# Kernel optimization log

Measured on AMD Instinct MI355X. Metric: run time of the kernel, lower is better.

## Reference

```python
import jax, jax.numpy as jnp
import numpy as np
import math
from jax import lax

CANVAS = 300.0
NUM_CLASSES = 80
SCORE_THR = 0.01
K_CAND = 400   # candidates kept per image before NMS (cfg cltop=400)
K_OUT = 200    # final detections per image
IOU_THR = 0.45
CLIP = math.log(1000.0 / 16.0)  # exp clamp in decode_boxes
_FSIZES = [38, 19, 10, 5, 3, 1]
_STRIDES = [8, 16, 32, 64, 100, 300]
_SCALES = [0.07, 0.15, 0.33, 0.51, 0.69, 0.87, 1.05]
_AR3 = [1, 2, 3]
_ANUMS = [4, 6, 6, 6, 4, 4]


def _make_priors():
    # SSD300 priors (tv config: no rounding, clamp to canvas), cxcywh, [8732,4]
    out = []
    for i, (st, fs) in enumerate(zip(_STRIDES, _FSIZES)):
        s = _SCALES[i] * 300.0
        e = math.sqrt(_SCALES[i] * _SCALES[i + 1]) * 300.0
        ratios = [2.0, 0.5] + ([3.0, 1.0 / 3.0] if i in _AR3 else [])
        wh = [(s, s), (e, e)] + [(s * math.sqrt(r), s / math.sqrt(r)) for r in ratios]
        wh = np.array([(min(w, 300.0), min(h, 300.0)) for w, h in wh], np.float32)
        cy, cx = np.meshgrid(np.arange(fs), np.arange(fs), indexing='ij')
        ctr = np.stack([(cx + 0.5) * st, (cy + 0.5) * st], -1).reshape(-1, 2).astype(np.float32)
        A = wh.shape[0]
        out.append(np.concatenate([np.repeat(ctr, A, 0), np.tile(wh, (fs * fs, 1))], 1))
    return np.concatenate(out, 0)


def _head(x, w, b, tl):
    # Conv2d(c, an*tl, 3, 1, 1) -> permute(0,2,3,1) -> reshape(B, -1, tl)
    y = lax.conv_general_dilated(x, w, (1, 1), [(1, 1), (1, 1)],
                                 dimension_numbers=('NCHW', 'OIHW', 'NCHW'))
    y = y + b[None, :, None, None]
    n = y.shape[0]
    return jnp.transpose(y, (0, 2, 3, 1)).reshape(n, -1, tl)


def _decode(deltas, pri):
    cx = pri[:, 0] + deltas[:, 0] * 0.1 * pri[:, 2]
    cy = pri[:, 1] + deltas[:, 1] * 0.1 * pri[:, 3]
    w = pri[:, 2] * jnp.exp(jnp.minimum(deltas[:, 2] * 0.2, CLIP))
    h = pri[:, 3] * jnp.exp(jnp.minimum(deltas[:, 3] * 0.2, CLIP))
    b = jnp.stack([cx - 0.5 * w, cy - 0.5 * h, cx + 0.5 * w, cy + 0.5 * h], -1)
    return jnp.clip(b, 0.0, CANVAS)  # clamp_to_canvas


def _pairwise_iou(b):
    area = (b[:, 2] - b[:, 0]) * (b[:, 3] - b[:, 1])
    lt = jnp.maximum(b[:, None, :2], b[None, :, :2])
    rb = jnp.minimum(b[:, None, 2:], b[None, :, 2:])
    wh = jnp.clip(rb - lt, 0.0)
    inter = wh[..., 0] * wh[..., 1]
    return inter / (area[:, None] + area[None, :] - inter + 1e-9)


def _post_one(scr, reg, priors):
    # scr [A, C] (background already dropped), reg [A, 4]
    C = scr.shape[1]
    flat = jnp.where(scr > SCORE_THR, scr, 0.0).reshape(-1)
    s, idx = lax.top_k(flat, K_CAND)          # sorted desc -> greedy NMS order
    cls = idx % C + 1                          # bckg_class_first=False -> +1
    anc = idx // C
    boxes = _decode(reg[anc], priors[anc])
    valid = (s > 0.0) & (boxes[:, 2] > boxes[:, 0]) & (boxes[:, 3] > boxes[:, 1])
    s = jnp.where(valid, s, 0.0)
    # class-aware NMS via per-class coordinate offset (batched_nms trick)
    off = cls.astype(boxes.dtype)[:, None] * (CANVAS + 1.0)
    iou = _pairwise_iou(boxes + off)
    def body(i, keep):
        sup = (iou[i] > IOU_THR) & (jnp.arange(K_CAND) > i) & keep[i]
        return keep & (~sup)
    keep = lax.fori_loop(0, K_CAND, body, valid)
    fs, fi = lax.top_k(jnp.where(keep, s, 0.0), K_OUT)
    return boxes[fi], fs, jnp.where(fs > 0.0, cls[fi], 0).astype(jnp.int32)


def setup_inputs() -> dict:
    key = jax.random.key(0)
    shapes = [(16, 512, 38, 38), (16, 1024, 19, 19), (16, 512, 10, 10),
              (16, 256, 5, 5), (16, 256, 3, 3), (16, 256, 1, 1)]
    d = {}
    k = key
    for i, (shp, an) in enumerate(zip(shapes, _ANUMS)):
        c = shp[1]
        k, k1, k2, k3 = jax.random.split(k, 4)
        d['feat%d' % i] = jax.random.normal(k1, shp, jnp.float32)
        d['cls_w%d' % i] = jax.random.normal(k2, (an * (NUM_CLASSES + 1), c, 3, 3), jnp.float32) * 0.03
        d['cls_b%d' % i] = jnp.zeros((an * (NUM_CLASSES + 1),), jnp.float32)
        d['reg_w%d' % i] = jax.random.normal(k3, (an * 4, c, 3, 3), jnp.float32) * 0.03
        d['reg_b%d' % i] = jnp.zeros((an * 4,), jnp.float32)
    d['priors'] = jnp.asarray(_make_priors())
    return d


def reference(feat0, feat1, feat2, feat3, feat4, feat5,
              cls_w0, cls_b0, cls_w1, cls_b1, cls_w2, cls_b2,
              cls_w3, cls_b3, cls_w4, cls_b4, cls_w5, cls_b5,
              reg_w0, reg_b0, reg_w1, reg_b1, reg_w2, reg_b2,
              reg_w3, reg_b3, reg_w4, reg_b4, reg_w5, reg_b5,
              priors):
    feats = [feat0, feat1, feat2, feat3, feat4, feat5]
    cws = [cls_w0, cls_w1, cls_w2, cls_w3, cls_w4, cls_w5]
    cbs = [cls_b0, cls_b1, cls_b2, cls_b3, cls_b4, cls_b5]
    rws = [reg_w0, reg_w1, reg_w2, reg_w3, reg_w4, reg_w5]
    rbs = [reg_b0, reg_b1, reg_b2, reg_b3, reg_b4, reg_b5]
    cls = jnp.concatenate([_head(f, w, b, NUM_CLASSES + 1) for f, w, b in zip(feats, cws, cbs)], 1)
    reg = jnp.concatenate([_head(f, w, b, 4) for f, w, b in zip(feats, rws, rbs)], 1)
    scr = jax.nn.softmax(cls, axis=-1)[:, :, 1:]  # drop background (class 0)
    boxes, scores, classes = jax.vmap(_post_one, in_axes=(0, 0, None))(scr, reg, priors)
    return boxes, scores, classes
```

## Files before the change

kernel.cpp:

```cpp
#include <hip/hip_runtime.h>
#include <math.h>
#include <stdint.h>

#define NIMG 16
#define A_TOTAL 8732
#define NCLS 80
#define TL_CLS 81
#define CANVASF 300.0f
#define SCORE_THR 0.01f
#define IOU_THRF 0.45f
#define KCAND 400
#define KOUT 200
#define CAND_CAP 4096
#define NBIN 65536

typedef double d4 __attribute__((ext_vector_type(4)));

__device__ __forceinline__ float clampf(float v, float lo, float hi) {
    return fminf(fmaxf(v, lo), hi);
}

struct ConvJobs {
    const float* feat[6];
    const float* wgtT[6];
    const float* biasC[6];
    const float* biasR[6];
    float* outc;
    float* outr;
    int Cin[6], lgC[6], Hd[6], Mtot[6], Mcls[6], Mp[6], an[6], off[6], cn[6];
    int mW[6], jobTiles[6];
    int cum[8][7];
    int cs[8][6];
};

struct TransJobs {
    const float* srcC[6];
    const float* srcR[6];
    float* dst[6];
    int Cin[6], K[6], Mcls[6], Mtot[6], Mp[6], mT[6], start[6];
    int total;
};

__global__ __launch_bounds__(256) void transpose_wgt(TransJobs tj)
{
    __shared__ float lds[32][33];
    int bid = (int)blockIdx.x;
    int L = 0;
    while (L + 1 < 6 && bid >= tj.start[L + 1]) L++;
    int rel = bid - tj.start[L];
    int mTi = rel % tj.mT[L];
    int kTi = rel / tj.mT[L];
    int m0 = mTi * 32, k0 = kTi * 32;
    const int K = tj.K[L];
    const int tid = threadIdx.x;

    {
        int ml = tid >> 3;
        int kq = (tid & 7) << 2;
        int m = m0 + ml;
        float4 v = make_float4(0.f, 0.f, 0.f, 0.f);
        if (m < tj.Mcls[L])
            v = *(const float4*)(tj.srcC[L] + (size_t)m * K + k0 + kq);
        else if (m < tj.Mtot[L])
            v = *(const float4*)(tj.srcR[L] + (size_t)(m - tj.Mcls[L]) * K + k0 + kq);
        lds[kq + 0][ml] = v.x;
        lds[kq + 1][ml] = v.y;
        lds[kq + 2][ml] = v.z;
        lds[kq + 3][ml] = v.w;
    }
    __syncthreads();
    {
        int kk = tid >> 3;
        int mq = (tid & 7) << 2;
        int k = k0 + kk;
        int ci = k / 9;
        int r = k - ci * 9;
        int kp = r * tj.Cin[L] + ci;
        float4 w;
        w.x = lds[kk][mq + 0];
        w.y = lds[kk][mq + 1];
        w.z = lds[kk][mq + 2];
        w.w = lds[kk][mq + 3];
        *(float4*)(tj.dst[L] + (size_t)kp * tj.Mp[L] + m0 + mq) = w;
    }
}

template<int CN>
__device__ __forceinline__ void conv_wave(
    const float* __restrict__ feat, const float* __restrict__ wgtT,
    const float* __restrict__ biasC, const float* __restrict__ biasR,
    float* __restrict__ outc, float* __restrict__ outr,
    int Cin, int lgC, int Hd, int Mtot, int Mcls, int Mp, int an, int lvl_off,
    int n0, int m0)
{
    const int K = Cin * 9;
    const int HW = Hd * Hd;
    const int N = NIMG * HW;
    const int CHW = Cin * HW;
    const int lane = threadIdx.x & 63;
    const int lm = lane & 15;
    const int lk = lane >> 4;

    int rowIdx[4], colIdx[4];
    {
        d4 z = (d4){0.0, 0.0, 0.0, 0.0};
        d4 pr = __builtin_amdgcn_mfma_f64_16x16x4f64((double)lm, 1.0, z, 0, 0, 0);
        d4 pc = __builtin_amdgcn_mfma_f64_16x16x4f64(1.0, (double)lm, z, 0, 0, 0);
#pragma unroll
        for (int i = 0; i < 4; i++) {
            rowIdx[i] = (int)(pr[i] * 0.25 + 0.5);
            colIdx[i] = (int)(pc[i] * 0.25 + 0.5);
        }
    }

    const int gPerR = Cin >> 2;
    const int KBg = K >> 2;

    int voffA = lk * Mp + m0 + lm;
    int voffB[CN];
    float maskc[CN];
    float bufA[2][2], bufB[2][CN], bufM[2][CN];

    d4 acc[2][CN];
#pragma unroll
    for (int a = 0; a < 2; a++)
#pragma unroll
        for (int c = 0; c < CN; c++) acc[a][c] = (d4){0.0, 0.0, 0.0, 0.0};

    auto newR = [&](int r) {
        int ky = (r * 171) >> 9;
        int kx = r - 3 * ky;
#pragma unroll
        for (int c = 0; c < CN; c++) {
            int ng = n0 + lm + 16 * c;
            bool nv = ng < N;
            int bimg = 0, p = 0;
            if (nv) { bimg = ng / HW; p = ng - bimg * HW; }
            int y0 = p / Hd;
            int x0 = p - y0 * Hd;
            int yy = y0 + ky - 1;
            int xx = x0 + kx - 1;
            bool v = nv && (yy >= 0) && (yy < Hd) && (xx >= 0) && (xx < Hd);
            maskc[c] = v ? 1.0f : 0.0f;
            voffB[c] = bimg * CHW + lk * HW + (v ? (yy * Hd + xx) : 0);
        }
    };

    auto loadG = [&](int g, int slot) {
        if ((g & (gPerR - 1)) == 0) newR(g >> (lgC - 2));
#pragma unroll
        for (int c = 0; c < CN; c++) {
            bufB[slot][c] = feat[voffB[c]];
            bufM[slot][c] = maskc[c];
            voffB[c] += 4 * HW;
        }
        bufA[slot][0] = wgtT[voffA];
        bufA[slot][1] = wgtT[voffA + 16];
        voffA += 4 * Mp;
    };

    loadG(0, 0);
    loadG(1, 1);
    for (int g = 0; g < KBg; g += 2) {
        {
            double a0 = (double)bufA[0][0];
            double a1 = (double)bufA[0][1];
            double bb[CN];
#pragma unroll
            for (int c = 0; c < CN; c++) bb[c] = (double)(bufB[0][c] * bufM[0][c]);
            if (g + 2 < KBg) loadG(g + 2, 0);
#pragma unroll
            for (int c = 0; c < CN; c++) {
                acc[0][c] = __builtin_amdgcn_mfma_f64_16x16x4f64(a0, bb[c], acc[0][c], 0, 0, 0);
                acc[1][c] = __builtin_amdgcn_mfma_f64_16x16x4f64(a1, bb[c], acc[1][c], 0, 0, 0);
            }
        }
        {
            double a0 = (double)bufA[1][0];
            double a1 = (double)bufA[1][1];
            double bb[CN];
#pragma unroll
            for (int c = 0; c < CN; c++) bb[c] = (double)(bufB[1][c] * bufM[1][c]);
            if (g + 3 < KBg) loadG(g + 3, 1);
#pragma unroll
            for (int c = 0; c < CN; c++) {
                acc[0][c] = __builtin_amdgcn_mfma_f64_16x16x4f64(a0, bb[c], acc[0][c], 0, 0, 0);
                acc[1][c] = __builtin_amdgcn_mfma_f64_16x16x4f64(a1, bb[c], acc[1][c], 0, 0, 0);
            }
        }
    }

#pragma unroll
    for (int mi2 = 0; mi2 < 2; mi2++)
#pragma unroll
    for (int c = 0; c < CN; c++)
#pragma unroll
    for (int i = 0; i < 4; i++) {
        int mg = m0 + mi2 * 16 + rowIdx[i];
        int ng2 = n0 + c * 16 + colIdx[i];
        if (mg >= Mtot || ng2 >= N) continue;
        int b = ng2 / HW;
        int p = ng2 - b * HW;
        double val = acc[mi2][c][i];
        if (mg < Mcls) {
            int aidx = mg / TL_CLS;
            int t = mg - aidx * TL_CLS;
            int row = lvl_off + p * an + aidx;
            outc[((size_t)b * A_TOTAL + row) * TL_CLS + t] = (float)(val + (double)biasC[mg]);
        } else {
            int rm = mg - Mcls;
            int aidx = rm >> 2;
            int t = rm & 3;
            int row = lvl_off + p * an + aidx;
            outr[((size_t)b * A_TOTAL + row) * 4 + t] = (float)(val + (double)biasR[rm]);
        }
    }
}

__global__ __launch_bounds__(256, 4) void fused_conv(ConvJobs J)
{
    int bid = (int)blockIdx.x;
    int x = bid & 7;
    int r = bid >> 3;
    if (r >= J.cum[x][6]) return;
    int j = 0;
    while (j + 1 < 6 && r >= J.cum[x][j + 1]) j++;
    int blkInJob = J.cs[x][j] + (r - J.cum[x][j]);

    int wave = threadIdx.x >> 6;
    int tile = blkInJob * 4 + wave;
    if (tile >= J.jobTiles[j]) return;
    int mt = tile % J.mW[j];
    int nt = tile / J.mW[j];

    if (J.cn[j] == 2)
        conv_wave<2>(J.feat[j], J.wgtT[j], J.biasC[j], J.biasR[j], J.outc, J.outr,
                     J.Cin[j], J.lgC[j], J.Hd[j], J.Mtot[j], J.Mcls[j], J.Mp[j],
                     J.an[j], J.off[j], nt * 32, mt * 32);
    else
        conv_wave<4>(J.feat[j], J.wgtT[j], J.biasC[j], J.biasR[j], J.outc, J.outr,
                     J.Cin[j], J.lgC[j], J.Hd[j], J.Mtot[j], J.Mcls[j], J.Mp[j],
                     J.an[j], J.off[j], nt * 64, mt * 32);
}

__global__ __launch_bounds__(256) void softmax_kernel(
    const float* __restrict__ cls, float* __restrict__ scr, int nrows)
{
    __shared__ float buf[64 * 81];
    __shared__ float inv[64];
    const int row0 = blockIdx.x * 64;
    const int tid = threadIdx.x;

    for (int i = tid; i < 64 * 81; i += 256) {
        int r = row0 + i / 81;
        buf[i] = (r < nrows) ? cls[(size_t)row0 * 81 + i] : 0.0f;
    }
    __syncthreads();
    if (tid < 64) {
        float m = -1e30f;
        for (int c = 0; c < 81; c++) m = fmaxf(m, buf[tid * 81 + c]);
        double md = (double)m;
        double ssum = 0.0;
        for (int c = 0; c < 81; c++) {
            double e = exp((double)buf[tid * 81 + c] - md);
            buf[tid * 81 + c] = (float)e;
            ssum += e;
        }
        inv[tid] = (float)(1.0 / ssum);
    }
    __syncthreads();
    for (int i = tid; i < 64 * 80; i += 256) {
        int r = i / 80;
        int c = i - r * 80;
        int gr = row0 + r;
        if (gr < nrows) scr[(size_t)gr * 80 + c] = buf[r * 81 + c + 1] * inv[r];
    }
}

__global__ void zero_kernel(unsigned int* __restrict__ p, int n)
{
    int i = blockIdx.x * blockDim.x + threadIdx.x;
    if (i < n) p[i] = 0u;
}

__global__ void hist_kernel(const float* __restrict__ scr, unsigned int* __restrict__ hist)
{
    const int per_img = A_TOTAL * NCLS;
    const size_t total = (size_t)NIMG * per_img;
    for (size_t i = (size_t)blockIdx.x * blockDim.x + threadIdx.x; i < total;
         i += (size_t)gridDim.x * blockDim.x) {
        float v = scr[i];
        if (v > SCORE_THR) {
            int img = (int)(i / per_img);
            unsigned int u = __float_as_uint(v);
            atomicAdd(&hist[img * NBIN + (u >> 16)], 1u);
        }
    }
}

__global__ __launch_bounds__(1024) void select_kernel(
    const unsigned int* __restrict__ hist, unsigned int* __restrict__ sel)
{
    __shared__ unsigned int vals[1024];
    __shared__ unsigned int red[1024];
    __shared__ int s_total, s_b0, s_done;
    const int img = blockIdx.x;
    const int tid = threadIdx.x;
    if (tid == 0) { s_total = 0; s_b0 = 0; s_done = 0; }
    __syncthreads();
    for (int c = 63; c >= 0; c--) {
        unsigned int h = hist[img * NBIN + c * 1024 + tid];
        vals[tid] = h;
        red[tid] = h;
        __syncthreads();
        for (int s = 512; s > 0; s >>= 1) {
            if (tid < s) red[tid] += red[tid + s];
            __syncthreads();
        }
        if (tid == 0 && !s_done) {
            if (s_total + (int)red[0] >= KCAND) {
                int cum = s_total;
                for (int tt = 1023; tt >= 0; tt--) {
                    cum += (int)vals[tt];
                    if (cum >= KCAND) { s_b0 = c * 1024 + tt; s_done = 1; break; }
                }
            } else {
                s_total += (int)red[0];
            }
        }
        __syncthreads();
        if (s_done) break;
    }
    if (tid == 0) sel[img] = (unsigned int)s_b0;
}

__global__ void gather_kernel(const float* __restrict__ scr,
                              const unsigned int* __restrict__ sel,
                              unsigned int* __restrict__ candcnt,
                              uint2* __restrict__ cand)
{
    const int per_img = A_TOTAL * NCLS;
    const size_t total = (size_t)NIMG * per_img;
    for (size_t i = (size_t)blockIdx.x * blockDim.x + threadIdx.x; i < total;
         i += (size_t)gridDim.x * blockDim.x) {
        float v = scr[i];
        if (v > SCORE_THR) {
            int img = (int)(i / per_img);
            unsigned int u = __float_as_uint(v);
            if ((u >> 16) >= sel[img]) {
                unsigned int pos = atomicAdd(&candcnt[img], 1u);
                if (pos < CAND_CAP) {
                    unsigned int ridx = (unsigned int)(i - (size_t)img * per_img);
                    cand[(size_t)img * CAND_CAP + pos] = make_uint2(u, ridx);
                }
            }
        }
    }
}

__global__ __launch_bounds__(1024) void nms_kernel(
    const uint2* __restrict__ cand, const unsigned int* __restrict__ candcnt,
    const float* __restrict__ reg_all, const float* __restrict__ priors,
    float* __restrict__ out)
{
    __shared__ unsigned long long key[CAND_CAP];
    __shared__ float s_sc[KCAND];
    __shared__ float s_bx[KCAND][4];
    __shared__ float s_ob[KCAND][4];
    __shared__ float s_ar[KCAND];
    __shared__ float s_cl[KCAND];
    __shared__ int s_keep[KCAND];
    __shared__ int s_fi[KOUT];

    const int img = blockIdx.x;
    const int tid = threadIdx.x;
    unsigned int craw = candcnt[img];
    const int cnt = (craw > CAND_CAP) ? CAND_CAP : (int)craw;

    for (int i = tid; i < CAND_CAP; i += 1024) {
        unsigned long long kv = 0ull;
        if (i < cnt) {
            uint2 e = cand[(size_t)img * CAND_CAP + i];
            kv = ((unsigned long long)e.x << 32) | (unsigned int)(~e.y);
        }
        key[i] = kv;
    }
    __syncthreads();

    for (int ksz = 2; ksz <= CAND_CAP; ksz <<= 1) {
        for (int jj = ksz >> 1; jj > 0; jj >>= 1) {
            for (int i = tid; i < CAND_CAP; i += 1024) {
                int p = i ^ jj;
                if (p > i) {
                    bool desc = ((i & ksz) == 0);
                    unsigned long long a = key[i];
                    unsigned long long b = key[p];
                    bool sw = desc ? (a < b) : (a > b);
                    if (sw) { key[i] = b; key[p] = a; }
                }
            }
            __syncthreads();
        }
    }

    const float CLIPF = 4.135166556742356f;
    if (tid < KCAND) {
        const int j = tid;
        float s = 0.0f;
        unsigned int idx = 0u;
        if (j < cnt) {
            unsigned long long kv = key[j];
            unsigned int bits = (unsigned int)(kv >> 32);
            idx = ~((unsigned int)kv);
            s = __uint_as_float(bits);
        }
        int anc = (int)(idx / NCLS);
        int cl = (int)(idx - (unsigned int)anc * NCLS) + 1;
        const float* d = reg_all + ((size_t)img * A_TOTAL + anc) * 4;
        const float* pr = priors + (size_t)anc * 4;
        float d0 = d[0], d1 = d[1], d2 = d[2], d3 = d[3];
        float p0 = pr[0], p1 = pr[1], p2 = pr[2], p3 = pr[3];
        float cx = p0 + d0 * 0.1f * p2;
        float cy = p1 + d1 * 0.1f * p3;
        float t2 = fminf(d2 * 0.2f, CLIPF);
        float t3 = fminf(d3 * 0.2f, CLIPF);
        float bw = p2 * (float)exp((double)t2);
        float bh = p3 * (float)exp((double)t3);
        float x1 = clampf(cx - 0.5f * bw, 0.0f, CANVASF);
        float y1 = clampf(cy - 0.5f * bh, 0.0f, CANVASF);
        float x2 = clampf(cx + 0.5f * bw, 0.0f, CANVASF);
        float y2 = clampf(cy + 0.5f * bh, 0.0f, CANVASF);
        bool valid = (s > 0.0f) && (x2 > x1) && (y2 > y1);
        s = valid ? s : 0.0f;
        float off = (float)cl * (CANVASF + 1.0f);
        float ox1 = x1 + off, oy1 = y1 + off, ox2 = x2 + off, oy2 = y2 + off;
        s_sc[j] = s;
        s_cl[j] = (float)cl;
        s_keep[j] = valid ? 1 : 0;
        s_bx[j][0] = x1; s_bx[j][1] = y1; s_bx[j][2] = x2; s_bx[j][3] = y2;
        s_ob[j][0] = ox1; s_ob[j][1] = oy1; s_ob[j][2] = ox2; s_ob[j][3] = oy2;
        s_ar[j] = (ox2 - ox1) * (oy2 - oy1);
    }
    __syncthreads();

    for (int i = 0; i < KCAND; i++) {
        int ki = s_keep[i];
        if (ki && tid < KCAND && tid > i) {
            float lx = fmaxf(s_ob[i][0], s_ob[tid][0]);
            float ly = fmaxf(s_ob[i][1], s_ob[tid][1]);
            float rx = fminf(s_ob[i][2], s_ob[tid][2]);
            float ry = fminf(s_ob[i][3], s_ob[tid][3]);
            float iw = fmaxf(rx - lx, 0.0f);
            float ih = fmaxf(ry - ly, 0.0f);
            float inter = iw * ih;
            float iou = inter / (s_ar[i] + s_ar[tid] - inter + 1e-9f);
            if (iou > IOU_THRF) s_keep[tid] = 0;
        }
        __syncthreads();
    }

    if (tid == 0) {
        int pos = 0;
        for (int j = 0; j < KCAND && pos < KOUT; j++)
            if (s_keep[j]) s_fi[pos++] = j;
        for (int j = 0; j < KCAND && pos < KOUT; j++)
            if (!s_keep[j]) s_fi[pos++] = j;
    }
    __syncthreads();

    if (tid < KOUT) {
        int j = s_fi[tid];
        float fs = s_keep[j] ? s_sc[j] : 0.0f;
        size_t o = (size_t)img * KOUT + tid;
        out[o * 4 + 0] = s_bx[j][0];
        out[o * 4 + 1] = s_bx[j][1];
        out[o * 4 + 2] = s_bx[j][2];
        out[o * 4 + 3] = s_bx[j][3];
        out[(size_t)NIMG * KOUT * 4 + o] = fs;
        out[(size_t)NIMG * KOUT * 5 + o] = (fs > 0.0f) ? s_cl[j] : 0.0f;
    }
}

extern "C" void kernel_launch(void* const* d_in, const int* in_sizes, int n_in,
                              void* d_out, int out_size, void* d_ws, size_t ws_size,
                              hipStream_t stream)
{
    static const int Cin_[6] = {512, 1024, 512, 256, 256, 256};
    static const int lgC_[6] = {9, 10, 9, 8, 8, 8};
    static const int HW_[6]  = {38, 19, 10, 5, 3, 1};
    static const int an_[6]  = {4, 6, 6, 6, 4, 4};
    static const int off_[6] = {0, 5776, 7942, 8542, 8692, 8728};
    static const int Mp_[6]  = {352, 512, 512, 512, 352, 352};
    static const size_t wOffF_[6] = {0, 1622016, 6340608, 8699904, 0, 9879552};

    char* ws = (char*)d_ws;
    const size_t OFF_CLS  = 0;
    const size_t OFF_SCR  = 45266688;
    const size_t OFF_REG  = 89974528;
    const size_t OFF_HIST = 92209920;
    const size_t OFF_CCNT = 96404224;
    const size_t OFF_SEL  = 96404288;
    const size_t OFF_CAND = 96404352;

    float* cls_all = (float*)(ws + OFF_CLS);
    float* scr     = (float*)(ws + OFF_SCR);
    float* reg_all = (float*)(ws + OFF_REG);
    unsigned int* hist    = (unsigned int*)(ws + OFF_HIST);
    unsigned int* candcnt = (unsigned int*)(ws + OFF_CCNT);
    unsigned int* sel     = (unsigned int*)(ws + OFF_SEL);
    uint2* cand           = (uint2*)(ws + OFF_CAND);

    float* wT = scr;
    float* hT = (float*)hist;

    {
        TransJobs tj;
        int ts = 0;
        for (int L = 0; L < 6; L++) {
            tj.srcC[L] = (const float*)d_in[L * 5 + 1];
            tj.srcR[L] = (const float*)d_in[L * 5 + 3];
            tj.dst[L] = (L == 4) ? hT : (wT + wOffF_[L]);
            tj.Cin[L] = Cin_[L];
            tj.K[L] = Cin_[L] * 9;
            tj.Mcls[L] = an_[L] * TL_CLS;
            tj.Mtot[L] = an_[L] * 85;
            tj.Mp[L] = Mp_[L];
            tj.mT[L] = Mp_[L] / 32;
            tj.start[L] = ts;
            ts += (Mp_[L] / 32) * (Cin_[L] * 9 / 32);
        }
        tj.total = ts;
        transpose_wgt<<<ts, 256, 0, stream>>>(tj);
    }

    ConvJobs jobs;
    static const int ord_lvl[6] = {1, 0, 2, 3, 4, 5};
    int Bj[6];
    for (int q = 0; q < 6; q++) {
        int L = ord_lvl[q];
        int an = an_[L];
        jobs.feat[q]  = (const float*)d_in[L * 5 + 0];
        jobs.wgtT[q]  = (L == 4) ? hT : (wT + wOffF_[L]);
        jobs.biasC[q] = (const float*)d_in[L * 5 + 2];
        jobs.biasR[q] = (const float*)d_in[L * 5 + 4];
        jobs.Cin[q]   = Cin_[L];
        jobs.lgC[q]   = lgC_[L];
        jobs.Hd[q]    = HW_[L];
        jobs.Mcls[q]  = an * TL_CLS;
        jobs.Mtot[q]  = an * 85;
        jobs.Mp[q]    = Mp_[L];
        jobs.an[q]    = an;
        jobs.off[q]   = off_[L];
        jobs.cn[q]    = (L == 1) ? 2 : 4;
        int N = NIMG * HW_[L] * HW_[L];
        int nstep = 16 * jobs.cn[q];
        int nT = (N + nstep - 1) / nstep;
        int mW = (jobs.Mtot[q] + 31) / 32;
        jobs.mW[q] = mW;
        jobs.jobTiles[q] = nT * mW;
        Bj[q] = (nT * mW + 3) / 4;
    }
    int maxT = 0;
    for (int x = 0; x < 8; x++) {
        int acc = 0;
        for (int q = 0; q < 6; q++) {
            int s = (int)(((long long)x * Bj[q]) / 8);
            int e = (int)(((long long)(x + 1) * Bj[q]) / 8);
            jobs.cs[x][q] = s;
            jobs.cum[x][q] = acc;
            acc += e - s;
        }
        jobs.cum[x][6] = acc;
        if (acc > maxT) maxT = acc;
    }
    jobs.outc = cls_all;
    jobs.outr = reg_all;

    fused_conv<<<8 * maxT, 256, 0, stream>>>(jobs);

    {
        int nz = NIMG * NBIN + 16 + 16;
        zero_kernel<<<(nz + 255) / 256, 256, 0, stream>>>(hist, nz);
    }

    softmax_kernel<<<(NIMG * A_TOTAL + 63) / 64, 256, 0, stream>>>(cls_all, scr, NIMG * A_TOTAL);
    hist_kernel<<<2048, 256, 0, stream>>>(scr, hist);
    select_kernel<<<NIMG, 1024, 0, stream>>>(hist, sel);
    gather_kernel<<<2048, 256, 0, stream>>>(scr, sel, candcnt, cand);
    nms_kernel<<<NIMG, 1024, 0, stream>>>(cand, candcnt, reg_all,
                                          (const float*)d_in[30], (float*)d_out);
}
```

Baseline: 3.769 ms.

## Reorder conv weight K layout, fuse histogram into softmax, parallelize select scan

```diff
diff --git a/kernel.cpp b/kernel.cpp
--- a/kernel.cpp
+++ b/kernel.cpp
@@ -27,7 +27,7 @@
     const float* biasR[6];
     float* outc;
     float* outr;
-    int Cin[6], lgC[6], Hd[6], Mtot[6], Mcls[6], Mp[6], an[6], off[6], cn[6];
+    int Cin[6], Hd[6], Mtot[6], Mcls[6], Mp[6], an[6], off[6], cn[6];
     int mW[6], jobTiles[6];
     int cum[8][7];
     int cs[8][6];
@@ -75,7 +75,7 @@
         int k = k0 + kk;
         int ci = k / 9;
         int r = k - ci * 9;
-        int kp = r * tj.Cin[L] + ci;
+        int kp = (ci >> 2) * 36 + r * 4 + (ci & 3);
         float4 w;
         w.x = lds[kk][mq + 0];
         w.y = lds[kk][mq + 1];
@@ -90,10 +90,9 @@
     const float* __restrict__ feat, const float* __restrict__ wgtT,
     const float* __restrict__ biasC, const float* __restrict__ biasR,
     float* __restrict__ outc, float* __restrict__ outr,
-    int Cin, int lgC, int Hd, int Mtot, int Mcls, int Mp, int an, int lvl_off,
+    int Cin, int Hd, int Mtot, int Mcls, int Mp, int an, int lvl_off,
     int n0, int m0)
 {
-    const int K = Cin * 9;
     const int HW = Hd * Hd;
     const int N = NIMG * HW;
     const int CHW = Cin * HW;
@@ -113,82 +112,90 @@
         }
     }
 
-    const int gPerR = Cin >> 2;
-    const int KBg = K >> 2;
+    int voffB[CN];
+    int bits[CN];
+#pragma unroll
+    for (int c = 0; c < CN; c++) {
+        int ng = n0 + lm + 16 * c;
+        bool nv = ng < N;
+        int bimg = 0, p = 0;
+        if (nv) { bimg = ng / HW; p = ng - bimg * HW; }
+        int y0 = p / Hd;
+        int x0 = p - y0 * Hd;
+        voffB[c] = nv ? (bimg * CHW + lk * HW + y0 * Hd + x0) : 0;
+        int b = nv ? 16 : 0;
+        if (y0 >= 1) b |= 1;
+        if (y0 <= Hd - 2) b |= 2;
+        if (x0 >= 1) b |= 4;
+        if (x0 <= Hd - 2) b |= 8;
+        bits[c] = b;
+    }
+
+    int tap[9];
+#pragma unroll
+    for (int r = 0; r < 9; r++) tap[r] = (r / 3 - 1) * Hd + (r % 3) - 1;
 
     int voffA = lk * Mp + m0 + lm;
-    int voffB[CN];
-    float maskc[CN];
-    float bufA[2][2], bufB[2][CN], bufM[2][CN];
-
+
+    float bufB[2][CN], bufM[2][CN], bufA[2][2];
     d4 acc[2][CN];
 #pragma unroll
     for (int a = 0; a < 2; a++)
 #pragma unroll
         for (int c = 0; c < CN; c++) acc[a][c] = (d4){0.0, 0.0, 0.0, 0.0};
 
-    auto newR = [&](int r) {
-        int ky = (r * 171) >> 9;
-        int kx = r - 3 * ky;
-#pragma unroll
-        for (int c = 0; c < CN; c++) {
-            int ng = n0 + lm + 16 * c;
-            bool nv = ng < N;
-            int bimg = 0, p = 0;
-            if (nv) { bimg = ng / HW; p = ng - bimg * HW; }
-            int y0 = p / Hd;
-            int x0 = p - y0 * Hd;
-            int yy = y0 + ky - 1;
-            int xx = x0 + kx - 1;
-            bool v = nv && (yy >= 0) && (yy < Hd) && (xx >= 0) && (xx < Hd);
-            maskc[c] = v ? 1.0f : 0.0f;
-            voffB[c] = bimg * CHW + lk * HW + (v ? (yy * Hd + xx) : 0);
-        }
-    };
-
-    auto loadG = [&](int g, int slot) {
-        if ((g & (gPerR - 1)) == 0) newR(g >> (lgC - 2));
-#pragma unroll
-        for (int c = 0; c < CN; c++) {
-            bufB[slot][c] = feat[voffB[c]];
-            bufM[slot][c] = maskc[c];
-            voffB[c] += 4 * HW;
-        }
-        bufA[slot][0] = wgtT[voffA];
-        bufA[slot][1] = wgtT[voffA + 16];
-        voffA += 4 * Mp;
-    };
-
-    loadG(0, 0);
-    loadG(1, 1);
-    for (int g = 0; g < KBg; g += 2) {
-        {
-            double a0 = (double)bufA[0][0];
-            double a1 = (double)bufA[0][1];
-            double bb[CN];
-#pragma unroll
-            for (int c = 0; c < CN; c++) bb[c] = (double)(bufB[0][c] * bufM[0][c]);
-            if (g + 2 < KBg) loadG(g + 2, 0);
-#pragma unroll
-            for (int c = 0; c < CN; c++) {
-                acc[0][c] = __builtin_amdgcn_mfma_f64_16x16x4f64(a0, bb[c], acc[0][c], 0, 0, 0);
-                acc[1][c] = __builtin_amdgcn_mfma_f64_16x16x4f64(a1, bb[c], acc[1][c], 0, 0, 0);
-            }
-        }
-        {
-            double a0 = (double)bufA[1][0];
-            double a1 = (double)bufA[1][1];
-            double bb[CN];
-#pragma unroll
-            for (int c = 0; c < CN; c++) bb[c] = (double)(bufB[1][c] * bufM[1][c]);
-            if (g + 3 < KBg) loadG(g + 3, 1);
-#pragma unroll
-            for (int c = 0; c < CN; c++) {
-                acc[0][c] = __builtin_amdgcn_mfma_f64_16x16x4f64(a0, bb[c], acc[0][c], 0, 0, 0);
-                acc[1][c] = __builtin_amdgcn_mfma_f64_16x16x4f64(a1, bb[c], acc[1][c], 0, 0, 0);
-            }
-        }
-    }
+#define CW_ISSUE(s_, r_)                                                       \
+    do {                                                                       \
+        const int R_ = 16 | (((r_) / 3 == 0) ? 1 : 0)                          \
+                          | (((r_) / 3 == 2) ? 2 : 0)                          \
+                          | (((r_) % 3 == 0) ? 4 : 0)                          \
+                          | (((r_) % 3 == 2) ? 8 : 0);                         \
+        _Pragma("unroll")                                                      \
+        for (int c2 = 0; c2 < CN; c2++) {                                      \
+            bool ok2 = (bits[c2] & R_) == R_;                                  \
+            bufM[s_][c2] = ok2 ? 1.0f : 0.0f;                                  \
+            bufB[s_][c2] = feat[voffB[c2] + (ok2 ? tap[r_] : 0)];              \
+        }                                                                      \
+        bufA[s_][0] = wgtT[voffA];                                             \
+        bufA[s_][1] = wgtT[voffA + 16];                                        \
+        voffA += 4 * Mp;                                                       \
+    } while (0)
+
+#define CW_BODY(u_, doIssue_)                                                  \
+    do {                                                                       \
+        const int s1 = (u_) & 1;                                               \
+        double a0_ = (double)bufA[s1][0];                                      \
+        double a1_ = (double)bufA[s1][1];                                      \
+        double bb_[CN];                                                        \
+        _Pragma("unroll")                                                      \
+        for (int c1 = 0; c1 < CN; c1++)                                        \
+            bb_[c1] = (double)(bufB[s1][c1] * bufM[s1][c1]);                   \
+        if (doIssue_) {                                                        \
+            if ((u_) == 7 || (u_) == 16) {                                     \
+                _Pragma("unroll")                                              \
+                for (int c1 = 0; c1 < CN; c1++) voffB[c1] += 4 * HW;           \
+            }                                                                  \
+            CW_ISSUE(s1, ((u_) + 2) % 9);                                      \
+        }                                                                      \
+        _Pragma("unroll")                                                      \
+        for (int c1 = 0; c1 < CN; c1++) {                                      \
+            acc[0][c1] = __builtin_amdgcn_mfma_f64_16x16x4f64(a0_, bb_[c1], acc[0][c1], 0, 0, 0); \
+            acc[1][c1] = __builtin_amdgcn_mfma_f64_16x16x4f64(a1_, bb_[c1], acc[1][c1], 0, 0, 0); \
+        }                                                                      \
+    } while (0)
+
+    const int CG = Cin >> 2;
+    CW_ISSUE(0, 0);
+    CW_ISSUE(1, 1);
+    for (int cg = 0; cg < CG - 2; cg += 2) {
+#pragma unroll
+        for (int u = 0; u < 18; u++) CW_BODY(u, true);
+    }
+#pragma unroll
+    for (int u = 0; u < 18; u++) CW_BODY(u, u < 16);
+
+#undef CW_BODY
+#undef CW_ISSUE
 
 #pragma unroll
     for (int mi2 = 0; mi2 < 2; mi2++)
@@ -235,16 +242,17 @@
 
     if (J.cn[j] == 2)
         conv_wave<2>(J.feat[j], J.wgtT[j], J.biasC[j], J.biasR[j], J.outc, J.outr,
-                     J.Cin[j], J.lgC[j], J.Hd[j], J.Mtot[j], J.Mcls[j], J.Mp[j],
+                     J.Cin[j], J.Hd[j], J.Mtot[j], J.Mcls[j], J.Mp[j],
                      J.an[j], J.off[j], nt * 32, mt * 32);
     else
         conv_wave<4>(J.feat[j], J.wgtT[j], J.biasC[j], J.biasR[j], J.outc, J.outr,
-                     J.Cin[j], J.lgC[j], J.Hd[j], J.Mtot[j], J.Mcls[j], J.Mp[j],
+                     J.Cin[j], J.Hd[j], J.Mtot[j], J.Mcls[j], J.Mp[j],
                      J.an[j], J.off[j], nt * 64, mt * 32);
 }
 
 __global__ __launch_bounds__(256) void softmax_kernel(
-    const float* __restrict__ cls, float* __restrict__ scr, int nrows)
+    const float* __restrict__ cls, float* __restrict__ scr,
+    unsigned int* __restrict__ hist, int nrows)
 {
     __shared__ float buf[64 * 81];
     __shared__ float inv[64];
@@ -273,7 +281,14 @@
         int r = i / 80;
         int c = i - r * 80;
         int gr = row0 + r;
-        if (gr < nrows) scr[(size_t)gr * 80 + c] = buf[r * 81 + c + 1] * inv[r];
+        if (gr < nrows) {
+            float v = buf[r * 81 + c + 1] * inv[r];
+            scr[(size_t)gr * 80 + c] = v;
+            if (v > SCORE_THR) {
+                int img = gr / A_TOTAL;
+                atomicAdd(&hist[img * NBIN + (__float_as_uint(v) >> 16)], 1u);
+            }
+        }
     }
 }
 
@@ -283,55 +298,42 @@
     if (i < n) p[i] = 0u;
 }
 
-__global__ void hist_kernel(const float* __restrict__ scr, unsigned int* __restrict__ hist)
-{
-    const int per_img = A_TOTAL * NCLS;
-    const size_t total = (size_t)NIMG * per_img;
-    for (size_t i = (size_t)blockIdx.x * blockDim.x + threadIdx.x; i < total;
-         i += (size_t)gridDim.x * blockDim.x) {
-        float v = scr[i];
-        if (v > SCORE_THR) {
-            int img = (int)(i / per_img);
-            unsigned int u = __float_as_uint(v);
-            atomicAdd(&hist[img * NBIN + (u >> 16)], 1u);
-        }
-    }
-}
-
 __global__ __launch_bounds__(1024) void select_kernel(
     const unsigned int* __restrict__ hist, unsigned int* __restrict__ sel)
 {
-    __shared__ unsigned int vals[1024];
-    __shared__ unsigned int red[1024];
-    __shared__ int s_total, s_b0, s_done;
+    __shared__ unsigned int ps[1024];
+    __shared__ int s_found;
     const int img = blockIdx.x;
     const int tid = threadIdx.x;
-    if (tid == 0) { s_total = 0; s_b0 = 0; s_done = 0; }
-    __syncthreads();
-    for (int c = 63; c >= 0; c--) {
-        unsigned int h = hist[img * NBIN + c * 1024 + tid];
-        vals[tid] = h;
-        red[tid] = h;
+
+    unsigned int p = 0;
+    const int base = img * NBIN + tid * 64;
+    for (int j = 0; j < 64; j++) p += hist[base + j];
+    ps[tid] = p;
+    if (tid == 0) s_found = 0;
+    __syncthreads();
+
+    for (int off = 1; off < 1024; off <<= 1) {
+        unsigned int v = (tid + off < 1024) ? ps[tid + off] : 0u;
         __syncthreads();
-        for (int s = 512; s > 0; s >>= 1) {
-            if (tid < s) red[tid] += red[tid + s];
-            __syncthreads();
-        }
-        if (tid == 0 && !s_done) {
-            if (s_total + (int)red[0] >= KCAND) {
-                int cum = s_total;
-                for (int tt = 1023; tt >= 0; tt--) {
-                    cum += (int)vals[tt];
-                    if (cum >= KCAND) { s_b0 = c * 1024 + tt; s_done = 1; break; }
-                }
-            } else {
-                s_total += (int)red[0];
-            }
-        }
+        ps[tid] += v;
         __syncthreads();
-        if (s_done) break;
-    }
-    if (tid == 0) sel[img] = (unsigned int)s_b0;
+    }
+
+    unsigned int St = ps[tid];
+    unsigned int Sn = (tid < 1023) ? ps[tid + 1] : 0u;
+    if (St >= KCAND && (tid == 1023 || Sn < KCAND)) {
+        unsigned int cum = Sn;
+        int b0 = 0;
+        for (int b = tid * 64 + 63; b >= tid * 64; b--) {
+            cum += hist[img * NBIN + b];
+            if (cum >= KCAND) { b0 = b; break; }
+        }
+        sel[img] = (unsigned int)b0;
+        s_found = 1;
+    }
+    __syncthreads();
+    if (tid == 0 && !s_found) sel[img] = 0u;
 }
 
 __global__ void gather_kernel(const float* __restrict__ scr,
@@ -486,12 +488,11 @@
                               hipStream_t stream)
 {
     static const int Cin_[6] = {512, 1024, 512, 256, 256, 256};
-    static const int lgC_[6] = {9, 10, 9, 8, 8, 8};
     static const int HW_[6]  = {38, 19, 10, 5, 3, 1};
     static const int an_[6]  = {4, 6, 6, 6, 4, 4};
     static const int off_[6] = {0, 5776, 7942, 8542, 8692, 8728};
     static const int Mp_[6]  = {352, 512, 512, 512, 352, 352};
-    static const size_t wOffF_[6] = {0, 1622016, 6340608, 8699904, 0, 9879552};
+    static const size_t wOffF_[6] = {0, 1624832, 6347520, 8710912, 0, 9894656};
 
     char* ws = (char*)d_ws;
     const size_t OFF_CLS  = 0;
@@ -544,7 +545,6 @@
         jobs.biasC[q] = (const float*)d_in[L * 5 + 2];
         jobs.biasR[q] = (const float*)d_in[L * 5 + 4];
         jobs.Cin[q]   = Cin_[L];
-        jobs.lgC[q]   = lgC_[L];
         jobs.Hd[q]    = HW_[L];
         jobs.Mcls[q]  = an * TL_CLS;
         jobs.Mtot[q]  = an * 85;
@@ -583,8 +583,8 @@
         zero_kernel<<<(nz + 255) / 256, 256, 0, stream>>>(hist, nz);
     }
 
-    softmax_kernel<<<(NIMG * A_TOTAL + 63) / 64, 256, 0, stream>>>(cls_all, scr, NIMG * A_TOTAL);
-    hist_kernel<<<2048, 256, 0, stream>>>(scr, hist);
+    softmax_kernel<<<(NIMG * A_TOTAL + 63) / 64, 256, 0, stream>>>(
+        cls_all, scr, hist, NIMG * A_TOTAL);
     select_kernel<<<NIMG, 1024, 0, stream>>>(hist, sel);
     gather_kernel<<<2048, 256, 0, stream>>>(scr, sel, candcnt, cand);
     nms_kernel<<<NIMG, 1024, 0, stream>>>(cand, candcnt, reg_all,
```

Result: slower. 5.227 ms (+38.7%).
